# Optimization experiments

Hardware: AMD Instinct MI355X
Metric: run time of the kernel (lower is better)

The kernel has to match this reference:

```python
import jax, jax.numpy as jnp
import numpy as np

EMBED = 1024
HEADS = 16
HEAD_DIM = EMBED // HEADS
LN_EPS = 1e-5


def setup_inputs() -> dict:
    key = jax.random.key(0)
    ks = jax.random.split(key, 12)
    B, LQ, LK = 2, 2048, 2048
    s = 1.0 / np.sqrt(EMBED)
    inp = {
        "query_seq": jax.random.normal(ks[0], (B, LQ, EMBED), jnp.float32),
        "key_value_seq": jax.random.normal(ks[1], (B, LK, EMBED), jnp.float32),
        "prompt_size": 0,
        "Wq": jax.random.normal(ks[2], (EMBED, EMBED), jnp.float32) * s,
        "bq": jnp.zeros((EMBED,), jnp.float32),
        "Wk": jax.random.normal(ks[3], (EMBED, EMBED), jnp.float32) * s,
        "bk": jnp.zeros((EMBED,), jnp.float32),
        "Wv": jax.random.normal(ks[4], (EMBED, EMBED), jnp.float32) * s,
        "bv": jnp.zeros((EMBED,), jnp.float32),
        "Wo": jax.random.normal(ks[5], (EMBED, EMBED), jnp.float32) * s,
        "bo": jnp.zeros((EMBED,), jnp.float32),
        "ln_gamma": jnp.ones((EMBED,), jnp.float32),
        "ln_beta": jnp.zeros((EMBED,), jnp.float32),
    }
    return inp


def _split_heads(x):
    B, L, _ = x.shape
    return x.reshape(B, L, HEADS, HEAD_DIM).transpose(0, 2, 1, 3)  # [B,H,L,Dh]


def reference(query_seq, key_value_seq, prompt_size, Wq, bq, Wk, bk, Wv, bv, Wo, bo, ln_gamma, ln_beta):
    # projections (torch nn.Linear: x @ W.T + b)
    q = _split_heads(query_seq @ Wq.T + bq)
    k = _split_heads(key_value_seq @ Wk.T + bk)
    v = _split_heads(key_value_seq @ Wv.T + bv)
    # naive attention: full score matrix, softmax over keys
    scores = jnp.einsum("bhqd,bhkd->bhqk", q, k) / np.sqrt(HEAD_DIM).astype(np.float32)
    attn = jax.nn.softmax(scores, axis=-1)
    ctx = jnp.einsum("bhqk,bhkd->bhqd", attn, v)
    B, H, LQ, Dh = ctx.shape
    ctx = ctx.transpose(0, 2, 1, 3).reshape(B, LQ, H * Dh)
    out = ctx @ Wo.T + bo
    # residual + LayerNorm
    x = out + query_seq
    mu = jnp.mean(x, axis=-1, keepdims=True)
    var = jnp.var(x, axis=-1, keepdims=True)
    return (x - mu) * jax.lax.rsqrt(var + LN_EPS) * ln_gamma + ln_beta
```

## Files before the change

kernel.cpp:

```cpp
#include <hip/hip_runtime.h>

typedef unsigned short u16;
typedef unsigned int u32;
typedef __attribute__((ext_vector_type(8))) __bf16 bf16x8;
typedef __attribute__((ext_vector_type(4))) float f32x4;
typedef __attribute__((ext_vector_type(16))) float f32x16;

#define EMBED 1024
#define NB 2
#define LQ 2048
#define HEADS 16
#define DH 64
#define QSCALE 0.18033688011112042f

__device__ __forceinline__ u16 f2bf(float f) {
  u32 u = __float_as_uint(f);
  u32 r = (u + 0x7FFFu + ((u >> 16) & 1u)) >> 16;
  return (u16)r;
}

__device__ __forceinline__ void glds16(const void* g, void* l) {
  __builtin_amdgcn_global_load_lds((const __attribute__((address_space(1))) void*)g,
                                   (__attribute__((address_space(3))) void*)l, 16, 0, 0);
}

__device__ __forceinline__ f32x4 mfma16(bf16x8 a, bf16x8 b, f32x4 c) {
  return __builtin_amdgcn_mfma_f32_16x16x32_bf16(a, b, c, 0, 0, 0);
}
__device__ __forceinline__ f32x16 mfma32(bf16x8 a, bf16x8 b, f32x16 c) {
  return __builtin_amdgcn_mfma_f32_32x32x16_bf16(a, b, c, 0, 0, 0);
}

__device__ __forceinline__ void pl32(u32& a, u32& b) {
  asm("v_permlane32_swap_b32 %0, %1" : "+v"(a), "+v"(b));
}

__device__ __forceinline__ u32 packbf(float a, float b) {
  return __builtin_amdgcn_perm(__float_as_uint(b), __float_as_uint(a), 0x07060302u);
}

__global__ __launch_bounds__(256) void cast_kernel(
    const float* __restrict__ q, const float* __restrict__ kv,
    const float* __restrict__ wq, const float* __restrict__ wk,
    const float* __restrict__ wv, const float* __restrict__ wo,
    u16* __restrict__ qb, u16* __restrict__ kvb, u16* __restrict__ wqb,
    u16* __restrict__ wkb, u16* __restrict__ wvb, u16* __restrict__ wob) {
  int bid = blockIdx.x;
  const float* src;
  u16* dst;
  long base;
  if (bid < 2048) {
    src = q; dst = qb; base = (long)bid * 2048;
  } else if (bid < 4096) {
    src = kv; dst = kvb; base = (long)(bid - 2048) * 2048;
  } else {
    int wsel = (bid - 4096) >> 9;
    int wb = (bid - 4096) & 511;
    if (wsel == 0) { src = wq; dst = wqb; }
    else if (wsel == 1) { src = wk; dst = wkb; }
    else if (wsel == 2) { src = wv; dst = wvb; }
    else { src = wo; dst = wob; }
    base = (long)wb * 2048;
  }
  long e = base + (long)threadIdx.x * 8;
  float4 f0 = *(const float4*)(src + e);
  float4 f1 = *(const float4*)(src + e + 4);
  uint4 o;
  o.x = (u32)f2bf(f0.x) | ((u32)f2bf(f0.y) << 16);
  o.y = (u32)f2bf(f0.z) | ((u32)f2bf(f0.w) << 16);
  o.z = (u32)f2bf(f1.x) | ((u32)f2bf(f1.y) << 16);
  o.w = (u32)f2bf(f1.z) | ((u32)f2bf(f1.w) << 16);
  *(uint4*)(dst + e) = o;
}

template <int IT>
__device__ __forceinline__ void gemm_core(
    u16* As, u16* Bs, const u16* __restrict__ A, const u16* __restrict__ W,
    const float* __restrict__ bias, const float* __restrict__ resid,
    void* __restrict__ outp, int mode, int bx, int by) {
  const int K = EMBED;
  const int TM = IT * 32;
  const int tid = threadIdx.x;
  const int lane = tid & 63;
  const int wv = tid >> 6;
  const int wm = wv >> 1, wn = wv & 1;
  const int l16 = lane & 15, quad = lane >> 4;
  const long tile_m = (long)bx * TM;
  const long tile_n = (long)by * 128;

  f32x4 z4 = {0.f, 0.f, 0.f, 0.f};
  f32x4 acc[IT][4];
#pragma unroll
  for (int i = 0; i < IT; i++)
#pragma unroll
    for (int j = 0; j < 4; j++) acc[i][j] = z4;

  for (int k0 = 0; k0 < K; k0 += 64) {
#pragma unroll
    for (int it = 0; it < TM / 32; it++) {
      int lin = it * 256 + tid;
      int row = lin >> 3, cc = lin & 7;
      glds16(A + (tile_m + row) * K + k0 + ((cc ^ (row & 7)) << 3), As + lin * 8);
    }
#pragma unroll
    for (int it = 0; it < 4; it++) {
      int lin = it * 256 + tid;
      int row = lin >> 3, cc = lin & 7;
      glds16(W + (tile_n + row) * K + k0 + ((cc ^ (row & 7)) << 3), Bs + lin * 8);
    }
    __syncthreads();
#pragma unroll
    for (int ki = 0; ki < 2; ki++) {
      bf16x8 af[IT], bfr[4];
#pragma unroll
      for (int i = 0; i < IT; i++) {
        int row = wm * (IT * 16) + i * 16 + l16;
        af[i] = *(const bf16x8*)(As + row * 64 + (((ki * 4 + quad) ^ (row & 7)) << 3));
      }
#pragma unroll
      for (int j = 0; j < 4; j++) {
        int row = wn * 64 + j * 16 + l16;
        bfr[j] = *(const bf16x8*)(Bs + row * 64 + (((ki * 4 + quad) ^ (row & 7)) << 3));
      }
#pragma unroll
      for (int i = 0; i < IT; i++)
#pragma unroll
        for (int j = 0; j < 4; j++) acc[i][j] = mfma16(af[i], bfr[j], acc[i][j]);
    }
    __syncthreads();
  }

#pragma unroll
  for (int j = 0; j < 4; j++) {
    int gn = (int)tile_n + wn * 64 + j * 16 + l16;
    float bv = bias[gn];
#pragma unroll
    for (int i = 0; i < IT; i++) {
      long gm0 = tile_m + wm * (IT * 16) + i * 16 + quad * 4;
      if (mode == 3) {
#pragma unroll
        for (int r = 0; r < 4; r++) {
          long idx = (gm0 + r) * EMBED + gn;
          ((float*)outp)[idx] = acc[i][j][r] + bv + resid[idx];
        }
      } else if (mode == 2) {
        int b = (int)(gm0 >> 11), l = (int)(gm0 & 2047);
        int hh = gn >> 6, dh = gn & 63;
        uint2 pk;
        pk.x = (u32)f2bf(acc[i][j][0] + bv) | ((u32)f2bf(acc[i][j][1] + bv) << 16);
        pk.y = (u32)f2bf(acc[i][j][2] + bv) | ((u32)f2bf(acc[i][j][3] + bv) << 16);
        *(uint2*)((u16*)outp + (long)((b * HEADS + hh) * DH + dh) * LQ + l) = pk;
      } else {
#pragma unroll
        for (int r = 0; r < 4; r++) {
          long gm = gm0 + r;
          float v = acc[i][j][r] + bv;
          if (mode == 0) v *= QSCALE;
          int b = (int)(gm >> 11), l = (int)(gm & 2047);
          int hh = gn >> 6, dh = gn & 63;
          ((u16*)outp)[(long)((b * HEADS + hh) * LQ + l) * DH + dh] = f2bf(v);
        }
      }
    }
  }
}

__global__ __launch_bounds__(256, 4) void qkv_kernel(
    const u16* __restrict__ qb, const u16* __restrict__ kvb,
    const u16* __restrict__ wqb, const u16* __restrict__ wkb, const u16* __restrict__ wvb,
    const float* __restrict__ bq, const float* __restrict__ bk, const float* __restrict__ bv,
    u16* __restrict__ Qh, u16* __restrict__ Kh, u16* __restrict__ Vt) {
  __shared__ u16 As[64 * 64];
  __shared__ u16 Bs[128 * 64];
  if (blockIdx.z == 0)      gemm_core<2>(As, Bs, qb,  wqb, bq, nullptr, Qh, 0, blockIdx.x, blockIdx.y);
  else if (blockIdx.z == 1) gemm_core<2>(As, Bs, kvb, wkb, bk, nullptr, Kh, 1, blockIdx.x, blockIdx.y);
  else                      gemm_core<2>(As, Bs, kvb, wvb, bv, nullptr, Vt, 2, blockIdx.x, blockIdx.y);
}

__global__ __launch_bounds__(256, 4) void oproj_kernel(
    const u16* __restrict__ ctx, const u16* __restrict__ wob,
    const float* __restrict__ bo, const float* __restrict__ resid, float* __restrict__ out) {
  __shared__ u16 As[64 * 64];
  __shared__ u16 Bs[128 * 64];
  gemm_core<2>(As, Bs, ctx, wob, bo, resid, out, 3, blockIdx.x, blockIdx.y);
}

__global__ __launch_bounds__(512, 4) void attn_kernel(
    const u16* __restrict__ Qh, const u16* __restrict__ Kh,
    const u16* __restrict__ Vt, u16* __restrict__ ctx) {
  __shared__ u16 KVs[4][2][64 * 64];
  const int tid = threadIdx.x;
  const int lane = tid & 63;
  const int wv = tid >> 6;
  const int qsub = wv >> 1;
  const int kh = wv & 1;
  const int l32 = lane & 31, h = lane >> 5;
  const int bid = (int)blockIdx.x;
  const int swz = (bid & 7) * 64 + (bid >> 3);
  const int bh = swz >> 4, qt = swz & 15;
  const long qoff = (long)bh * (LQ * DH) + (long)qt * (128 * DH);
  const long koff = (long)bh * (LQ * DH);
  const long voff = (long)bh * (DH * LQ);
  const int qbase = qsub * 32;
  const int krow = kh * 32 + l32;

#define STAGE_KV(t, N)                                                          \
  do {                                                                          \
    int row = tid >> 3, cc = tid & 7;                                           \
    glds16(Kh + koff + (long)((t) * 64 + row) * 64 + ((cc ^ (row & 7)) << 3),   \
           &KVs[N][0][0] + tid * 8);                                            \
    glds16(Vt + voff + (long)row * LQ + (t) * 64 + ((cc ^ (row & 7)) << 3),     \
           &KVs[N][1][0] + tid * 8);                                            \
  } while (0)

#define SYNC(W)                                                                 \
  do {                                                                          \
    asm volatile("s_waitcnt vmcnt(" #W ")" ::: "memory");                       \
    __builtin_amdgcn_s_barrier();                                               \
    asm volatile("" ::: "memory");                                              \
  } while (0)

  bf16x8 bq[4];
  {
    const u16* qp = Qh + qoff + (qbase + l32) * 64 + h * 8;
#pragma unroll
    for (int ks = 0; ks < 4; ks++) bq[ks] = *(const bf16x8*)(qp + ks * 16);
  }

  STAGE_KV(0, 0);
  STAGE_KV(1, 1);
  STAGE_KV(2, 2);
  SYNC(2);

  f32x16 z16 = {0.f, 0.f, 0.f, 0.f, 0.f, 0.f, 0.f, 0.f,
                0.f, 0.f, 0.f, 0.f, 0.f, 0.f, 0.f, 0.f};
  f32x16 ot[2];
  ot[0] = z16;
  ot[1] = z16;
  f32x16 st;
  uint2 pk[4];
  float2 ls2 = {0.f, 0.f};

#define DO_S(C)                                                                  \
  do {                                                                           \
    __builtin_amdgcn_s_setprio(1);                                               \
    _Pragma("unroll") for (int ks = 0; ks < 4; ks++) {                           \
      bf16x8 ak = *(const bf16x8*)(&KVs[C][0][0] + krow * 64 +                   \
                                   (((ks * 2 + h) ^ (krow & 7)) << 3));          \
      st = mfma32(ak, bq[ks], (ks == 0) ? z16 : st);                             \
    }                                                                            \
    __builtin_amdgcn_s_setprio(0);                                               \
  } while (0)

#define DO_SM()                                                                  \
  do {                                                                           \
    _Pragma("unroll") for (int g = 0; g < 4; g++) {                              \
      float p0 = __builtin_amdgcn_exp2f(st[g * 4 + 0]);                          \
      float p1 = __builtin_amdgcn_exp2f(st[g * 4 + 1]);                          \
      float p2 = __builtin_amdgcn_exp2f(st[g * 4 + 2]);                          \
      float p3 = __builtin_amdgcn_exp2f(st[g * 4 + 3]);                          \
      ls2.x += p0 + p2;                                                          \
      ls2.y += p1 + p3;                                                          \
      pk[g].x = packbf(p0, p1);                                                  \
      pk[g].y = packbf(p2, p3);                                                  \
    }                                                                            \
  } while (0)

#define DO_PV(P)                                                                 \
  do {                                                                           \
    _Pragma("unroll") for (int s = 0; s < 2; s++) {                              \
      uint2 wa = pk[s * 2];                                                      \
      uint2 wb = pk[s * 2 + 1];                                                  \
      u32 a0 = wa.x, b0 = wb.x, a1 = wa.y, b1 = wb.y;                            \
      pl32(a0, b0);                                                              \
      pl32(a1, b1);                                                              \
      union { u32 u[4]; bf16x8 v; } bp;                                          \
      bp.u[0] = a0;                                                              \
      bp.u[1] = a1;                                                              \
      bp.u[2] = b0;                                                              \
      bp.u[3] = b1;                                                              \
      __builtin_amdgcn_s_setprio(1);                                             \
      _Pragma("unroll") for (int mt2 = 0; mt2 < 2; mt2++) {                      \
        int row = mt2 * 32 + l32;                                                \
        int c = ((2 * kh + s) << 1) + h;                                         \
        bf16x8 av = *(const bf16x8*)(&KVs[P][1][0] + row * 64 +                  \
                                     ((c ^ (row & 7)) << 3));                    \
        ot[mt2] = mfma32(av, bp.v, ot[mt2]);                                     \
      }                                                                          \
      __builtin_amdgcn_s_setprio(0);                                             \
    }                                                                            \
  } while (0)

#define AITER(kt, P, C, N, W)                                                    \
  do {                                                                           \
    if ((kt) + 2 < 32) STAGE_KV((kt) + 2, N);                                    \
    DO_SM();                                                                     \
    DO_S(C);                                                                     \
    DO_PV(P);                                                                    \
    SYNC(W);                                                                     \
  } while (0)

  DO_S(0);

  AITER(1, 0, 1, 3, 2);
  for (int k0 = 2; k0 < 30; k0 += 4) {
    AITER(k0 + 0, 1, 2, 0, 2);
    AITER(k0 + 1, 2, 3, 1, 2);
    AITER(k0 + 2, 3, 0, 2, 2);
    AITER(k0 + 3, 0, 1, 3, 2);
  }
  AITER(30, 1, 2, 0, 0);
  AITER(31, 2, 3, 1, 0);
  DO_SM();
  DO_PV(3);

#undef STAGE_KV
#undef SYNC
#undef DO_S
#undef DO_SM
#undef DO_PV
#undef AITER

  float lsum = ls2.x + ls2.y;
  lsum += __shfl_xor(lsum, 32);

  float* mrgf = (float*)(&KVs[0][0][0]);
  float* mlsf = mrgf + 4 * 64 * 36;
  __syncthreads();
  if (kh == 1) {
    int mbase = (qsub * 64 + lane) * 36;
#pragma unroll
    for (int mt2 = 0; mt2 < 2; mt2++)
#pragma unroll
      for (int e = 0; e < 16; e++) mrgf[mbase + mt2 * 16 + e] = ot[mt2][e];
    mlsf[qsub * 64 + lane] = lsum;
  }
  __syncthreads();
  if (kh == 0) {
    int mbase = (qsub * 64 + lane) * 36;
    lsum += mlsf[qsub * 64 + lane];
    float inv = 1.0f / lsum;
    const int b = bh >> 4, head = bh & 15;
    int qrow = qt * 128 + qbase + l32;
    long base = (long)(b * LQ + qrow) * EMBED + head * DH;
#pragma unroll
    for (int mt2 = 0; mt2 < 2; mt2++) {
#pragma unroll
      for (int g = 0; g < 4; g++) {
        float o0 = (ot[mt2][g * 4 + 0] + mrgf[mbase + mt2 * 16 + g * 4 + 0]) * inv;
        float o1 = (ot[mt2][g * 4 + 1] + mrgf[mbase + mt2 * 16 + g * 4 + 1]) * inv;
        float o2 = (ot[mt2][g * 4 + 2] + mrgf[mbase + mt2 * 16 + g * 4 + 2]) * inv;
        float o3 = (ot[mt2][g * 4 + 3] + mrgf[mbase + mt2 * 16 + g * 4 + 3]) * inv;
        uint2 pkk;
        pkk.x = (u32)f2bf(o0) | ((u32)f2bf(o1) << 16);
        pkk.y = (u32)f2bf(o2) | ((u32)f2bf(o3) << 16);
        *(uint2*)(ctx + base + mt2 * 32 + g * 8 + 4 * h) = pkk;
      }
    }
  }
}

__global__ __launch_bounds__(256) void ln_kernel(
    float* __restrict__ x, const float* __restrict__ gamma, const float* __restrict__ beta) {
  __shared__ float red[8];
  const int tid = threadIdx.x;
  const long row = blockIdx.x;
  float4 v = *(const float4*)(x + row * EMBED + tid * 4);
  float s = v.x + v.y + v.z + v.w;
  float sq = v.x * v.x + v.y * v.y + v.z * v.z + v.w * v.w;
#pragma unroll
  for (int off = 1; off < 64; off <<= 1) {
    s += __shfl_xor(s, off);
    sq += __shfl_xor(sq, off);
  }
  if ((tid & 63) == 0) {
    red[(tid >> 6) * 2] = s;
    red[(tid >> 6) * 2 + 1] = sq;
  }
  __syncthreads();
  s = red[0] + red[2] + red[4] + red[6];
  sq = red[1] + red[3] + red[5] + red[7];
  float mu = s * (1.f / EMBED);
  float var = sq * (1.f / EMBED) - mu * mu;
  float rstd = rsqrtf(var + 1e-5f);
  float4 g = *(const float4*)(gamma + tid * 4);
  float4 bt = *(const float4*)(beta + tid * 4);
  float4 ov;
  ov.x = (v.x - mu) * rstd * g.x + bt.x;
  ov.y = (v.y - mu) * rstd * g.y + bt.y;
  ov.z = (v.z - mu) * rstd * g.z + bt.z;
  ov.w = (v.w - mu) * rstd * g.w + bt.w;
  *(float4*)(x + row * EMBED + tid * 4) = ov;
}

extern "C" void kernel_launch(void* const* d_in, const int* in_sizes, int n_in,
                              void* d_out, int out_size, void* d_ws, size_t ws_size,
                              hipStream_t stream) {
  const float* q     = (const float*)d_in[0];
  const float* kv    = (const float*)d_in[1];
  const float* Wq    = (const float*)d_in[3];
  const float* bq    = (const float*)d_in[4];
  const float* Wk    = (const float*)d_in[5];
  const float* bk    = (const float*)d_in[6];
  const float* Wv    = (const float*)d_in[7];
  const float* bv    = (const float*)d_in[8];
  const float* Wo    = (const float*)d_in[9];
  const float* bo    = (const float*)d_in[10];
  const float* gamma = (const float*)d_in[11];
  const float* beta  = (const float*)d_in[12];

  char* ws = (char*)d_ws;
  u16* qb  = (u16*)(ws + (0l  << 20));
  u16* kvb = (u16*)(ws + (8l  << 20));
  u16* wqb = (u16*)(ws + (16l << 20));
  u16* wkb = (u16*)(ws + (18l << 20));
  u16* wvb = (u16*)(ws + (20l << 20));
  u16* wob = (u16*)(ws + (22l << 20));
  u16* Qh  = (u16*)(ws + (24l << 20));
  u16* Kh  = (u16*)(ws + (32l << 20));
  u16* Vt  = (u16*)(ws + (40l << 20));
  u16* ctx = (u16*)(ws + (48l << 20));
  float* out = (float*)d_out;

  cast_kernel<<<6144, 256, 0, stream>>>(q, kv, Wq, Wk, Wv, Wo, qb, kvb, wqb, wkb, wvb, wob);
  qkv_kernel<<<dim3(64, 8, 3), 256, 0, stream>>>(qb, kvb, wqb, wkb, wvb, bq, bk, bv, Qh, Kh, Vt);
  attn_kernel<<<512, 512, 0, stream>>>(Qh, Kh, Vt, ctx);
  oproj_kernel<<<dim3(64, 8), 256, 0, stream>>>(ctx, wob, bo, q, out);
  ln_kernel<<<4096, 256, 0, stream>>>(out, gamma, beta);
}
```

Measured before the change: 206.2 us.

## Swap GEMM operand roles for vectorized epilogue stores and use wave-per-row LayerNorm

The Q, K and output projections now compute the transposed product, with the weight as the M operand and activations as N. Each lane then holds four consecutive output features, so the epilogue does packed 8-byte bf16 stores and float4 residual loads and stores instead of scalar ones. The grid mapping is changed to match, and V keeps the original orientation. LayerNorm now gives each wave one row and drops the shared-memory reduction and barrier; it runs fewer blocks with more loads per thread.

After: 211.0 us. +2.3%, slower.

```diff
diff --git a/kernel.cpp b/kernel.cpp
--- a/kernel.cpp
+++ b/kernel.cpp
@@ -130,36 +130,59 @@
     __syncthreads();
   }
 
-#pragma unroll
-  for (int j = 0; j < 4; j++) {
-    int gn = (int)tile_n + wn * 64 + j * 16 + l16;
-    float bv = bias[gn];
-#pragma unroll
-    for (int i = 0; i < IT; i++) {
-      long gm0 = tile_m + wm * (IT * 16) + i * 16 + quad * 4;
-      if (mode == 3) {
-#pragma unroll
-        for (int r = 0; r < 4; r++) {
-          long idx = (gm0 + r) * EMBED + gn;
-          ((float*)outp)[idx] = acc[i][j][r] + bv + resid[idx];
-        }
-      } else if (mode == 2) {
+  if (mode == 2) {
+#pragma unroll
+    for (int j = 0; j < 4; j++) {
+      int gn = (int)tile_n + wn * 64 + j * 16 + l16;
+      float bv = bias[gn];
+#pragma unroll
+      for (int i = 0; i < IT; i++) {
+        long gm0 = tile_m + wm * (IT * 16) + i * 16 + quad * 4;
         int b = (int)(gm0 >> 11), l = (int)(gm0 & 2047);
         int hh = gn >> 6, dh = gn & 63;
         uint2 pk;
         pk.x = (u32)f2bf(acc[i][j][0] + bv) | ((u32)f2bf(acc[i][j][1] + bv) << 16);
         pk.y = (u32)f2bf(acc[i][j][2] + bv) | ((u32)f2bf(acc[i][j][3] + bv) << 16);
         *(uint2*)((u16*)outp + (long)((b * HEADS + hh) * DH + dh) * LQ + l) = pk;
-      } else {
-#pragma unroll
-        for (int r = 0; r < 4; r++) {
-          long gm = gm0 + r;
-          float v = acc[i][j][r] + bv;
-          if (mode == 0) v *= QSCALE;
-          int b = (int)(gm >> 11), l = (int)(gm & 2047);
-          int hh = gn >> 6, dh = gn & 63;
-          ((u16*)outp)[(long)((b * HEADS + hh) * LQ + l) * DH + dh] = f2bf(v);
-        }
+      }
+    }
+  } else if (mode == 3) {
+#pragma unroll
+    for (int i = 0; i < IT; i++) {
+      int o0 = (int)tile_m + wm * (IT * 16) + i * 16 + quad * 4;
+      float b0 = bias[o0 + 0], b1 = bias[o0 + 1];
+      float b2 = bias[o0 + 2], b3 = bias[o0 + 3];
+#pragma unroll
+      for (int j = 0; j < 4; j++) {
+        int l = (int)tile_n + wn * 64 + j * 16 + l16;
+        long idx = (long)l * EMBED + o0;
+        float4 rv = *(const float4*)(resid + idx);
+        float4 ov;
+        ov.x = acc[i][j][0] + b0 + rv.x;
+        ov.y = acc[i][j][1] + b1 + rv.y;
+        ov.z = acc[i][j][2] + b2 + rv.z;
+        ov.w = acc[i][j][3] + b3 + rv.w;
+        *(float4*)((float*)outp + idx) = ov;
+      }
+    }
+  } else {
+#pragma unroll
+    for (int i = 0; i < IT; i++) {
+      int o0 = (int)tile_m + wm * (IT * 16) + i * 16 + quad * 4;
+      int hh = o0 >> 6, dh = o0 & 63;
+      float b0 = bias[o0 + 0], b1 = bias[o0 + 1];
+      float b2 = bias[o0 + 2], b3 = bias[o0 + 3];
+#pragma unroll
+      for (int j = 0; j < 4; j++) {
+        int l = (int)tile_n + wn * 64 + j * 16 + l16;
+        int b = l >> 11, ll = l & 2047;
+        float v0 = acc[i][j][0] + b0, v1 = acc[i][j][1] + b1;
+        float v2 = acc[i][j][2] + b2, v3 = acc[i][j][3] + b3;
+        if (mode == 0) { v0 *= QSCALE; v1 *= QSCALE; v2 *= QSCALE; v3 *= QSCALE; }
+        uint2 pk;
+        pk.x = (u32)f2bf(v0) | ((u32)f2bf(v1) << 16);
+        pk.y = (u32)f2bf(v2) | ((u32)f2bf(v3) << 16);
+        *(uint2*)((u16*)outp + (long)((b * HEADS + hh) * LQ + ll) * DH + dh) = pk;
       }
     }
   }
@@ -172,9 +195,10 @@
     u16* __restrict__ Qh, u16* __restrict__ Kh, u16* __restrict__ Vt) {
   __shared__ u16 As[64 * 64];
   __shared__ u16 Bs[128 * 64];
-  if (blockIdx.z == 0)      gemm_core<2>(As, Bs, qb,  wqb, bq, nullptr, Qh, 0, blockIdx.x, blockIdx.y);
-  else if (blockIdx.z == 1) gemm_core<2>(As, Bs, kvb, wkb, bk, nullptr, Kh, 1, blockIdx.x, blockIdx.y);
-  else                      gemm_core<2>(As, Bs, kvb, wvb, bv, nullptr, Vt, 2, blockIdx.x, blockIdx.y);
+  int id = blockIdx.x, z = blockIdx.y;
+  if (z == 0)      gemm_core<2>(As, Bs, wqb, qb,  bq, nullptr, Qh, 0, id & 15, id >> 4);
+  else if (z == 1) gemm_core<2>(As, Bs, wkb, kvb, bk, nullptr, Kh, 1, id & 15, id >> 4);
+  else             gemm_core<2>(As, Bs, kvb, wvb, bv, nullptr, Vt, 2, id & 63, id >> 6);
 }
 
 __global__ __launch_bounds__(256, 4) void oproj_kernel(
@@ -182,7 +206,7 @@
     const float* __restrict__ bo, const float* __restrict__ resid, float* __restrict__ out) {
   __shared__ u16 As[64 * 64];
   __shared__ u16 Bs[128 * 64];
-  gemm_core<2>(As, Bs, ctx, wob, bo, resid, out, 3, blockIdx.x, blockIdx.y);
+  gemm_core<2>(As, Bs, wob, ctx, bo, resid, out, 3, blockIdx.x, blockIdx.y);
 }
 
 __global__ __launch_bounds__(512, 4) void attn_kernel(
@@ -362,35 +386,37 @@
 
 __global__ __launch_bounds__(256) void ln_kernel(
     float* __restrict__ x, const float* __restrict__ gamma, const float* __restrict__ beta) {
-  __shared__ float red[8];
-  const int tid = threadIdx.x;
-  const long row = blockIdx.x;
-  float4 v = *(const float4*)(x + row * EMBED + tid * 4);
-  float s = v.x + v.y + v.z + v.w;
-  float sq = v.x * v.x + v.y * v.y + v.z * v.z + v.w * v.w;
+  const int lane = threadIdx.x & 63;
+  const int wid = threadIdx.x >> 6;
+  const long row = (long)blockIdx.x * 4 + wid;
+  float* xr = x + row * EMBED;
+  float4 v[4];
+  float s = 0.f, sq = 0.f;
+#pragma unroll
+  for (int k = 0; k < 4; k++) {
+    v[k] = *(const float4*)(xr + k * 256 + lane * 4);
+    s += v[k].x + v[k].y + v[k].z + v[k].w;
+    sq += v[k].x * v[k].x + v[k].y * v[k].y + v[k].z * v[k].z + v[k].w * v[k].w;
+  }
 #pragma unroll
   for (int off = 1; off < 64; off <<= 1) {
     s += __shfl_xor(s, off);
     sq += __shfl_xor(sq, off);
   }
-  if ((tid & 63) == 0) {
-    red[(tid >> 6) * 2] = s;
-    red[(tid >> 6) * 2 + 1] = sq;
-  }
-  __syncthreads();
-  s = red[0] + red[2] + red[4] + red[6];
-  sq = red[1] + red[3] + red[5] + red[7];
   float mu = s * (1.f / EMBED);
   float var = sq * (1.f / EMBED) - mu * mu;
   float rstd = rsqrtf(var + 1e-5f);
-  float4 g = *(const float4*)(gamma + tid * 4);
-  float4 bt = *(const float4*)(beta + tid * 4);
-  float4 ov;
-  ov.x = (v.x - mu) * rstd * g.x + bt.x;
-  ov.y = (v.y - mu) * rstd * g.y + bt.y;
-  ov.z = (v.z - mu) * rstd * g.z + bt.z;
-  ov.w = (v.w - mu) * rstd * g.w + bt.w;
-  *(float4*)(x + row * EMBED + tid * 4) = ov;
+#pragma unroll
+  for (int k = 0; k < 4; k++) {
+    float4 g = *(const float4*)(gamma + k * 256 + lane * 4);
+    float4 bt = *(const float4*)(beta + k * 256 + lane * 4);
+    float4 ov;
+    ov.x = (v[k].x - mu) * rstd * g.x + bt.x;
+    ov.y = (v[k].y - mu) * rstd * g.y + bt.y;
+    ov.z = (v[k].z - mu) * rstd * g.z + bt.z;
+    ov.w = (v[k].w - mu) * rstd * g.w + bt.w;
+    *(float4*)(xr + k * 256 + lane * 4) = ov;
+  }
 }
 
 extern "C" void kernel_launch(void* const* d_in, const int* in_sizes, int n_in,
@@ -423,8 +449,8 @@
   float* out = (float*)d_out;
 
   cast_kernel<<<6144, 256, 0, stream>>>(q, kv, Wq, Wk, Wv, Wo, qb, kvb, wqb, wkb, wvb, wob);
-  qkv_kernel<<<dim3(64, 8, 3), 256, 0, stream>>>(qb, kvb, wqb, wkb, wvb, bq, bk, bv, Qh, Kh, Vt);
+  qkv_kernel<<<dim3(512, 3), 256, 0, stream>>>(qb, kvb, wqb, wkb, wvb, bq, bk, bv, Qh, Kh, Vt);
   attn_kernel<<<512, 512, 0, stream>>>(Qh, Kh, Vt, ctx);
-  oproj_kernel<<<dim3(64, 8), 256, 0, stream>>>(ctx, wob, bo, q, out);
-  ln_kernel<<<4096, 256, 0, stream>>>(out, gamma, beta);
-}
+  oproj_kernel<<<dim3(16, 32), 256, 0, stream>>>(ctx, wob, bo, q, out);
+  ln_kernel<<<1024, 256, 0, stream>>>(out, gamma, beta);
+}
```

## Triple-buffer GEMM K-loop with async LDS loads and vmcnt-based barriers

Applied to the files above, without the earlier changes.

Rewrites the projection GEMM mainloop from a single-buffered 64-wide K step with two barriers per step into a 3-stage ring of 32-wide K slices. Global-to-LDS loads for stage t+2 are issued before computing stage t, with an explicit s_waitcnt vmcnt plus barrier per step. The LDS swizzle is adjusted for 32-column rows. The aim is to hide global load latency behind MFMA work, at the cost of a finer K step, more barriers overall, and a hand-counted waitcnt schedule that must match the number of outstanding loads.

Measured after the change: 224.2 us. +8.7%, slower.

```diff
diff --git a/kernel.cpp b/kernel.cpp
--- a/kernel.cpp
+++ b/kernel.cpp
@@ -75,7 +75,7 @@
 
 template <int IT>
 __device__ __forceinline__ void gemm_core(
-    u16* As, u16* Bs, const u16* __restrict__ A, const u16* __restrict__ W,
+    u16* AsB, u16* BsB, const u16* __restrict__ A, const u16* __restrict__ W,
     const float* __restrict__ bias, const float* __restrict__ resid,
     void* __restrict__ outp, int mode, int bx, int by) {
   const int K = EMBED;
@@ -95,40 +95,70 @@
 #pragma unroll
     for (int j = 0; j < 4; j++) acc[i][j] = z4;
 
-  for (int k0 = 0; k0 < K; k0 += 64) {
-#pragma unroll
-    for (int it = 0; it < TM / 32; it++) {
-      int lin = it * 256 + tid;
-      int row = lin >> 3, cc = lin & 7;
-      glds16(A + (tile_m + row) * K + k0 + ((cc ^ (row & 7)) << 3), As + lin * 8);
-    }
-#pragma unroll
-    for (int it = 0; it < 4; it++) {
-      int lin = it * 256 + tid;
-      int row = lin >> 3, cc = lin & 7;
-      glds16(W + (tile_n + row) * K + k0 + ((cc ^ (row & 7)) << 3), Bs + lin * 8);
-    }
-    __syncthreads();
-#pragma unroll
-    for (int ki = 0; ki < 2; ki++) {
-      bf16x8 af[IT], bfr[4];
-#pragma unroll
-      for (int i = 0; i < IT; i++) {
-        int row = wm * (IT * 16) + i * 16 + l16;
-        af[i] = *(const bf16x8*)(As + row * 64 + (((ki * 4 + quad) ^ (row & 7)) << 3));
-      }
-#pragma unroll
-      for (int j = 0; j < 4; j++) {
-        int row = wn * 64 + j * 16 + l16;
-        bfr[j] = *(const bf16x8*)(Bs + row * 64 + (((ki * 4 + quad) ^ (row & 7)) << 3));
-      }
-#pragma unroll
-      for (int i = 0; i < IT; i++)
-#pragma unroll
-        for (int j = 0; j < 4; j++) acc[i][j] = mfma16(af[i], bfr[j], acc[i][j]);
-    }
-    __syncthreads();
-  }
+#define GSTAGE(t, S)                                                            \
+  do {                                                                          \
+    _Pragma("unroll") for (int it2 = 0; it2 < (TM * 4) / 256; it2++) {          \
+      int lin = it2 * 256 + tid;                                                \
+      int row = lin >> 2, cc = lin & 3;                                         \
+      glds16(A + (tile_m + row) * K + (t) * 32 +                                \
+                 ((cc ^ ((row >> 1) & 3)) << 3),                                \
+             AsB + (S) * (TM * 32) + lin * 8);                                  \
+    }                                                                           \
+    _Pragma("unroll") for (int it2 = 0; it2 < 2; it2++) {                       \
+      int lin = it2 * 256 + tid;                                                \
+      int row = lin >> 2, cc = lin & 3;                                         \
+      glds16(W + (tile_n + row) * K + (t) * 32 +                                \
+                 ((cc ^ ((row >> 1) & 3)) << 3),                                \
+             BsB + (S) * (128 * 32) + lin * 8);                                 \
+    }                                                                           \
+  } while (0)
+
+#define GCOMP(S)                                                                \
+  do {                                                                          \
+    bf16x8 af[IT], bfr[4];                                                      \
+    _Pragma("unroll") for (int i = 0; i < IT; i++) {                            \
+      int row = wm * (IT * 16) + i * 16 + l16;                                  \
+      af[i] = *(const bf16x8*)(AsB + (S) * (TM * 32) + row * 32 +               \
+                               ((quad ^ ((row >> 1) & 3)) << 3));               \
+    }                                                                           \
+    _Pragma("unroll") for (int j = 0; j < 4; j++) {                             \
+      int row = wn * 64 + j * 16 + l16;                                         \
+      bfr[j] = *(const bf16x8*)(BsB + (S) * (128 * 32) + row * 32 +             \
+                                ((quad ^ ((row >> 1) & 3)) << 3));              \
+    }                                                                           \
+    _Pragma("unroll") for (int i = 0; i < IT; i++)                              \
+      _Pragma("unroll") for (int j = 0; j < 4; j++)                             \
+          acc[i][j] = mfma16(af[i], bfr[j], acc[i][j]);                         \
+  } while (0)
+
+#define GSYNC(W_)                                                               \
+  do {                                                                          \
+    asm volatile("s_waitcnt vmcnt(" #W_ ")" ::: "memory");                      \
+    __builtin_amdgcn_s_barrier();                                               \
+    asm volatile("" ::: "memory");                                              \
+  } while (0)
+
+  GSTAGE(0, 0);
+  GSTAGE(1, 1);
+  GSYNC(3);
+  for (int t0 = 0; t0 < 30; t0 += 3) {
+    GSTAGE(t0 + 2, 2);
+    GCOMP(0);
+    GSYNC(3);
+    GSTAGE(t0 + 3, 0);
+    GCOMP(1);
+    GSYNC(3);
+    GSTAGE(t0 + 4, 1);
+    GCOMP(2);
+    GSYNC(3);
+  }
+  GCOMP(0);
+  GSYNC(0);
+  GCOMP(1);
+
+#undef GSTAGE
+#undef GCOMP
+#undef GSYNC
 
 #pragma unroll
   for (int j = 0; j < 4; j++) {
@@ -170,8 +200,8 @@
     const u16* __restrict__ wqb, const u16* __restrict__ wkb, const u16* __restrict__ wvb,
     const float* __restrict__ bq, const float* __restrict__ bk, const float* __restrict__ bv,
     u16* __restrict__ Qh, u16* __restrict__ Kh, u16* __restrict__ Vt) {
-  __shared__ u16 As[64 * 64];
-  __shared__ u16 Bs[128 * 64];
+  __shared__ u16 As[3 * 64 * 32];
+  __shared__ u16 Bs[3 * 128 * 32];
   if (blockIdx.z == 0)      gemm_core<2>(As, Bs, qb,  wqb, bq, nullptr, Qh, 0, blockIdx.x, blockIdx.y);
   else if (blockIdx.z == 1) gemm_core<2>(As, Bs, kvb, wkb, bk, nullptr, Kh, 1, blockIdx.x, blockIdx.y);
   else                      gemm_core<2>(As, Bs, kvb, wvb, bv, nullptr, Vt, 2, blockIdx.x, blockIdx.y);
@@ -180,8 +210,8 @@
 __global__ __launch_bounds__(256, 4) void oproj_kernel(
     const u16* __restrict__ ctx, const u16* __restrict__ wob,
     const float* __restrict__ bo, const float* __restrict__ resid, float* __restrict__ out) {
-  __shared__ u16 As[64 * 64];
-  __shared__ u16 Bs[128 * 64];
+  __shared__ u16 As[3 * 64 * 32];
+  __shared__ u16 Bs[3 * 128 * 32];
   gemm_core<2>(As, Bs, ctx, wob, bo, resid, out, 3, blockIdx.x, blockIdx.y);
 }
 
```
